# Kernel optimization log

Measured on AMD Instinct MI355X. Metric: run time of the kernel, lower is better.

The kernel has to match this reference:

```python
import jax, jax.numpy as jnp
import numpy as np

NUM_HEADS = 16
HEAD_DIM = 128
ROTARY_DIM = 32  # head_dim * rotary_pct(0.25)
ROPE_BASE = 10000.0
SCALE = HEAD_DIM ** -0.5


def _rotate_half(x):
    x1, x2 = jnp.split(x, 2, axis=-1)
    return jnp.concatenate((-x2, x1), axis=-1)


def _rope_tables(seq_len, dtype):
    inv_freq = 1.0 / (ROPE_BASE ** (jnp.arange(0, ROTARY_DIM, 2, dtype=jnp.float32) / ROTARY_DIM))
    freqs = jnp.arange(seq_len, dtype=jnp.float32)[:, None] * inv_freq[None, :]  # [S, rd/2]
    emb = jnp.concatenate((freqs, freqs), axis=-1)  # [S, rd]
    return jnp.cos(emb).astype(dtype), jnp.sin(emb).astype(dtype)


def setup_inputs() -> dict:
    key = jax.random.key(0)
    k1, k2, k3 = jax.random.split(key, 3)
    B, S, H = 2, 2048, 2048
    hidden_states = jax.random.normal(k1, (B, S, H), dtype=jnp.float32)
    attention_mask = jnp.zeros((B, 1, S, S), dtype=jnp.float32)
    Wqkv = jax.random.normal(k2, (H, 3 * H), dtype=jnp.float32) * (H ** -0.5)
    Wout = jax.random.normal(k3, (H, H), dtype=jnp.float32) * (H ** -0.5)
    return {"hidden_states": hidden_states, "attention_mask": attention_mask,
            "Wqkv": Wqkv, "Wout": Wout}


def reference(hidden_states, attention_mask, Wqkv, Wout):
    B, S, H = hidden_states.shape
    qkv = jnp.einsum('bsh,hk->bsk', hidden_states, Wqkv)  # [B,S,3H]
    q, k, v = jnp.split(qkv, 3, axis=-1)

    def to_heads(x):
        return x.reshape(B, S, NUM_HEADS, HEAD_DIM).transpose(0, 2, 1, 3)  # [B,nh,S,hd]

    q, k, v = to_heads(q), to_heads(k), to_heads(v)

    cos, sin = _rope_tables(S, hidden_states.dtype)  # [S, ROTARY_DIM]
    cos = cos[None, None, :, :]
    sin = sin[None, None, :, :]

    def rope(x):
        xr = x[..., :ROTARY_DIM]
        xr = xr * cos + _rotate_half(xr) * sin
        return jnp.concatenate((xr, x[..., ROTARY_DIM:]), axis=-1)

    q, k = rope(q), rope(k)

    scores = jnp.einsum('bhqd,bhkd->bhqk', q, k) * SCALE + attention_mask
    probs = jax.nn.softmax(scores, axis=-1)  # dropout p=0 -> identity
    ctx = jnp.einsum('bhqk,bhkd->bhqd', probs, v)
    ctx = ctx.transpose(0, 2, 1, 3).reshape(B, S, H)
    return jnp.einsum('bsh,ho->bso', ctx, Wout)
```

## Files before the change

### kernel.cpp

```cpp
#include <hip/hip_runtime.h>

typedef __attribute__((ext_vector_type(4))) float f32x4;
typedef __attribute__((ext_vector_type(8))) short s16x8;
typedef __attribute__((ext_vector_type(4))) unsigned short u16x4;
typedef __attribute__((ext_vector_type(8))) unsigned short u16x8;

#define DEVINL __device__ __forceinline__

constexpr int Bb = 2;
constexpr int Ss = 2048;
constexpr int Hh = 2048;
constexpr int NH = 16;
constexpr int HD = 128;
constexpr float ATT_SCALE = 0.08838834764831845f;
constexpr float CEXP = ATT_SCALE * 1.44269504089f;
constexpr float INV_SCALE = 11.313708498984761f;
constexpr float RAW_THR = 90.50966799f;

DEVINL unsigned short f2bf(float f) {
    unsigned u = __float_as_uint(f);
    u += 0x7FFFu + ((u >> 16) & 1u);
    return (unsigned short)(u >> 16);
}
DEVINL float bf2f(unsigned short h) { return __uint_as_float(((unsigned)h) << 16); }
DEVINL float fexp2(float x) { return __builtin_amdgcn_exp2f(x); }

DEVINL void gl16(const void* g, void* l) {
    __builtin_amdgcn_global_load_lds((const __attribute__((address_space(1))) void*)g,
                                     (__attribute__((address_space(3))) void*)l, 16, 0, 0);
}

__global__ void zero_flag_k(int* f) { if (threadIdx.x == 0) *f = 0; }

__global__ void scan_mask_k(const float* __restrict__ m, int* __restrict__ flag) {
    size_t i = ((size_t)blockIdx.x * 256 + threadIdx.x) * 4;
    f32x4 v = *(const f32x4*)(m + i);
    int any = (v[0] != 0.f) || (v[1] != 0.f) || (v[2] != 0.f) || (v[3] != 0.f);
    if (__any(any)) { if ((threadIdx.x & 63) == 0) atomicOr(flag, 1); }
}

__global__ void convH_k(const float* __restrict__ x, unsigned short* __restrict__ y) {
    size_t i = (size_t)blockIdx.x * 256 + threadIdx.x;
    f32x4 a = *(const f32x4*)(x + i * 8);
    f32x4 b = *(const f32x4*)(x + i * 8 + 4);
    u16x8 o;
    o[0] = f2bf(a[0]); o[1] = f2bf(a[1]); o[2] = f2bf(a[2]); o[3] = f2bf(a[3]);
    o[4] = f2bf(b[0]); o[5] = f2bf(b[1]); o[6] = f2bf(b[2]); o[7] = f2bf(b[3]);
    *(u16x8*)(y + i * 8) = o;
}

__global__ void convT_k(const float* __restrict__ W, unsigned short* __restrict__ Wt,
                        int R, int C) {
    __shared__ float tile[32][33];
    int c0 = blockIdx.x * 32, r0 = blockIdx.y * 32;
    int t = threadIdx.x;
    int rr = t >> 3, cc = (t & 7) * 4;
    f32x4 v = *(const f32x4*)(W + (size_t)(r0 + rr) * C + c0 + cc);
    tile[rr][cc + 0] = v[0]; tile[rr][cc + 1] = v[1];
    tile[rr][cc + 2] = v[2]; tile[rr][cc + 3] = v[3];
    __syncthreads();
    u16x4 o;
    o[0] = f2bf(tile[cc + 0][rr]); o[1] = f2bf(tile[cc + 1][rr]);
    o[2] = f2bf(tile[cc + 2][rr]); o[3] = f2bf(tile[cc + 3][rr]);
    *(u16x4*)(Wt + (size_t)(c0 + rr) * R + r0 + cc) = o;
}

#define PH(buf, kh, ih, sbuf, sunit, st, vm)                                      \
  {                                                                               \
    const char* Ar = lds + (buf)*65536;                                           \
    const char* Br = Ar + 32768;                                                  \
    s16x8 af[4];                                                                  \
    if ((ih) == 0) {                                                              \
      _Pragma("unroll")                                                           \
      for (int j = 0; j < 4; ++j) {                                               \
        int row = wn*64 + j*16 + lr;                                              \
        bfr[j] = *(const s16x8*)(Br + row*128 + (((kh)*64 + lg*16) ^ ((row&7)<<4))); \
      }                                                                           \
    }                                                                             \
    _Pragma("unroll")                                                             \
    for (int i = 0; i < 4; ++i) {                                                 \
      int row = wm*128 + (ih)*64 + i*16 + lr;                                     \
      af[i] = *(const s16x8*)(Ar + row*128 + (((kh)*64 + lg*16) ^ ((row&7)<<4))); \
    }                                                                             \
    STG(sbuf, sunit, st);                                                         \
    __builtin_amdgcn_s_barrier();                                                 \
    __builtin_amdgcn_sched_barrier(0);                                            \
    asm volatile("s_waitcnt lgkmcnt(0)" ::: "memory");                            \
    __builtin_amdgcn_sched_barrier(0);                                            \
    __builtin_amdgcn_s_setprio(1);                                                \
    _Pragma("unroll")                                                             \
    for (int i = 0; i < 4; ++i)                                                   \
      _Pragma("unroll")                                                           \
      for (int j = 0; j < 4; ++j)                                                 \
        acc[(ih)*4 + i][j] = __builtin_amdgcn_mfma_f32_16x16x32_bf16(             \
            af[i], bfr[j], acc[(ih)*4 + i][j], 0, 0, 0);                          \
    __builtin_amdgcn_s_setprio(0);                                                \
    if ((vm) >= 0) { asm volatile("s_waitcnt vmcnt(2)" ::: "memory"); }           \
    __builtin_amdgcn_sched_barrier(0);                                            \
    __builtin_amdgcn_s_barrier();                                                 \
    __builtin_amdgcn_sched_barrier(0);                                            \
  }

template<int MODE>
__global__ __launch_bounds__(512, 2)
void gemm256_k(const unsigned short* __restrict__ A, const unsigned short* __restrict__ Bt,
               float* __restrict__ Cf, unsigned short* __restrict__ Cb,
               int M, int N, int K) {
    __shared__ char lds[131072];
    int t = threadIdx.x, w = t >> 6, ln = t & 63, lr = ln & 15, lg = ln >> 4;
    int wm = w >> 2, wn = w & 3;
    int f = blockIdx.x, cpx = gridDim.x >> 3;
    int s = (f & 7) * cpx + (f >> 3);
    int nbn = N >> 8;
    int nb = s % nbn, mb = s / nbn;
    int m0 = mb * 256, n0 = nb * 256;
    const char* Ab = (const char*)A;
    const char* Bbp = (const char*)Bt;

    f32x4 acc[8][4];
#pragma unroll
    for (int i = 0; i < 8; ++i)
#pragma unroll
        for (int j = 0; j < 4; ++j) { acc[i][j][0] = 0.f; acc[i][j][1] = 0.f; acc[i][j][2] = 0.f; acc[i][j][3] = 0.f; }

    auto STG = [&](int sbuf, int unit, int kt) {
        int isB = unit >> 1;
        const char* src = isB ? Bbp : Ab;
        int rbase = isB ? n0 : m0;
        char* reg = lds + sbuf * 65536 + isB * 32768;
        size_t kb = ((size_t)kt * 64) * 2;
#pragma unroll
        for (int rr = 0; rr < 2; ++rr) {
            int rowbase = isB ? ((unit & 1) * 128 + rr * 64)
                              : (rr * 128 + (unit & 1) * 64);
            int row = rowbase + (t >> 3);
            int slot = (t & 7) ^ (row & 7);
            gl16(src + ((size_t)(rbase + row) * K) * 2 + kb + slot * 16,
                 reg + rowbase * 128 + t * 16);
        }
    };

    const int NT = K >> 6;
    STG(0, 0, 0); STG(0, 2, 0); STG(0, 3, 0); STG(0, 1, 0);
    STG(1, 0, 1);
    asm volatile("s_waitcnt vmcnt(2)" ::: "memory");
    __builtin_amdgcn_sched_barrier(0);
    __builtin_amdgcn_s_barrier();
    __builtin_amdgcn_sched_barrier(0);

    s16x8 bfr[4];
    for (int it = 0; it < (NT >> 1); ++it) {
        int e = it * 2;
        int e2 = (e + 2 < NT) ? e + 2 : e;
        int e3 = (e + 3 < NT) ? e + 3 : e + 1;
        PH(0, 0, 0,  1, 2, e + 1, -1)
        PH(0, 0, 1,  1, 3, e + 1, -1)
        PH(0, 1, 0,  1, 1, e + 1, -1)
        PH(0, 1, 1,  0, 0, e2,    1)
        PH(1, 0, 0,  0, 2, e2,   -1)
        PH(1, 0, 1,  0, 3, e2,   -1)
        PH(1, 1, 0,  0, 1, e2,   -1)
        PH(1, 1, 1,  1, 0, e3,    1)
    }
    asm volatile("s_waitcnt vmcnt(0)" ::: "memory");

    if (MODE == 0 && n0 < 4096 && (wn & 1) == 0) {
        float invf = fexp2((float)lr * -0.83048202372f);
#pragma unroll
        for (int i = 0; i < 8; ++i)
#pragma unroll
            for (int r = 0; r < 4; ++r) {
                int srow = (m0 + wm * 128 + i * 16 + lg * 4 + r) & (Ss - 1);
                float sn, cs;
                sincosf((float)srow * invf, &sn, &cs);
                float x1 = acc[i][0][r], x2 = acc[i][1][r];
                acc[i][0][r] = x1 * cs - x2 * sn;
                acc[i][1][r] = x2 * cs + x1 * sn;
            }
    }

#pragma unroll
    for (int i = 0; i < 8; ++i)
#pragma unroll
        for (int j = 0; j < 4; ++j)
#pragma unroll
            for (int r = 0; r < 4; ++r) {
                int gr = m0 + wm * 128 + i * 16 + lg * 4 + r;
                int gc = n0 + wn * 64 + j * 16 + lr;
                float vv = acc[i][j][r];
                if (MODE == 1) Cf[(size_t)gr * N + gc] = vv;
                else           Cb[(size_t)gr * N + gc] = f2bf(vv);
            }
}

__global__ void vtrans_k(const unsigned short* __restrict__ qkv, unsigned short* __restrict__ Vt) {
    __shared__ unsigned short tile[64][40];
    int bh = blockIdx.x; int b = bh >> 4, h = bh & 15;
    int s0 = blockIdx.y * 64, d0 = blockIdx.z * 32;
    int t = threadIdx.x;
    int r = t >> 2, c8 = (t & 3) * 8;
    u16x8 v = *(const u16x8*)(qkv + ((size_t)(b * Ss + s0 + r)) * 6144 + 4096 + h * 128 + d0 + c8);
#pragma unroll
    for (int e = 0; e < 8; ++e) tile[r][c8 + e] = v[e];
    __syncthreads();
    int dr = t >> 3, sc = (t & 7) * 8;
    u16x8 o;
#pragma unroll
    for (int e = 0; e < 8; ++e) o[e] = tile[sc + e][dr];
    *(u16x8*)(Vt + ((size_t)bh * HD + d0 + dr) * Ss + s0 + sc) = o;
}

__global__ __launch_bounds__(512)
void attn_k(const unsigned short* __restrict__ qkv, const unsigned short* __restrict__ Vt,
            const float* __restrict__ mask, unsigned short* __restrict__ ctxb,
            const int* __restrict__ flag) {
    __shared__ char ldsK[64 * 256];
    __shared__ char ldsV[128 * 128];
    __shared__ unsigned short ldsP[8][1024];
    int f = blockIdx.x;
    int swzb = (f & 7) * 64 + (f >> 3);
    int bh = swzb >> 4, qt = swzb & 15;
    int b = bh >> 4, h = bh & 15;
    int t = threadIdx.x, w = t >> 6, ln = t & 63, lr = ln & 15, lg = ln >> 4;
    int useMask = *flag;
    int qw0 = qt * 128 + w * 16;
    const char* qkvB = (const char*)qkv;
    const char* VtB = (const char*)Vt;

    s16x8 qf[4];
    size_t qbase = ((size_t)(b * Ss + qw0 + lr)) * 6144 + h * 128;
#pragma unroll
    for (int kc = 0; kc < 4; ++kc) qf[kc] = *(const s16x8*)(qkv + qbase + kc * 32 + lg * 8);

    float mr = -3e38f, lsum = 0.f;
    f32x4 ctxa[8];
#pragma unroll
    for (int dn = 0; dn < 8; ++dn) { ctxa[dn][0] = 0.f; ctxa[dn][1] = 0.f; ctxa[dn][2] = 0.f; ctxa[dn][3] = 0.f; }
    const float* mrow = mask + (size_t)b * Ss * Ss;

    for (int kk0 = 0; kk0 < Ss; kk0 += 64) {
        __syncthreads();
#pragma unroll
        for (int c = 0; c < 2; ++c) {
            int ci = c * 512 + t;
            int krow = ci >> 4, kcb = (ci & 15) << 4;
            gl16(qkvB + (((size_t)(b * Ss + kk0 + krow)) * 6144 + 2048 + h * 128) * 2 + (kcb ^ ((krow & 7) << 4)),
                 ldsK + ci * 16);
            int vrow = ci >> 3, vcb = (ci & 7) << 4;
            gl16(VtB + (((size_t)(bh * 128 + vrow)) * 2048 + kk0) * 2 + (vcb ^ ((vrow & 7) << 4)),
                 ldsV + ci * 16);
        }
        __syncthreads();

        f32x4 st[4];
#pragma unroll
        for (int n = 0; n < 4; ++n) {
            f32x4 sacc = {0.f, 0.f, 0.f, 0.f};
            const char* kb = ldsK + (n * 16 + lr) * 256;
            int sw = (lr & 7) << 4;
#pragma unroll
            for (int kc = 0; kc < 4; ++kc) {
                s16x8 kf = *(const s16x8*)(kb + ((kc * 64 + lg * 16) ^ sw));
                sacc = __builtin_amdgcn_mfma_f32_16x16x32_bf16(kf, qf[kc], sacc, 0, 0, 0);
            }
            st[n] = sacc;
        }
        if (useMask) {
#pragma unroll
            for (int n = 0; n < 4; ++n)
#pragma unroll
                for (int r = 0; r < 4; ++r)
                    st[n][r] += mrow[(size_t)(qw0 + lr) * Ss + kk0 + n * 16 + lg * 4 + r] * INV_SCALE;
        }
        float pmax = st[0][0];
#pragma unroll
        for (int n = 0; n < 4; ++n)
#pragma unroll
            for (int r = 0; r < 4; ++r) pmax = fmaxf(pmax, st[n][r]);
        pmax = fmaxf(pmax, __shfl_xor(pmax, 16));
        pmax = fmaxf(pmax, __shfl_xor(pmax, 32));
        bool need = pmax > mr + RAW_THR;
        if (__any(need)) {
            float mn = fmaxf(mr, pmax);
            float al = fexp2((mr - mn) * CEXP);
            mr = mn;
            lsum *= al;
            float a0 = __shfl(al, lg * 4 + 0), a1 = __shfl(al, lg * 4 + 1);
            float a2 = __shfl(al, lg * 4 + 2), a3 = __shfl(al, lg * 4 + 3);
#pragma unroll
            for (int dn = 0; dn < 8; ++dn) {
                ctxa[dn][0] *= a0; ctxa[dn][1] *= a1; ctxa[dn][2] *= a2; ctxa[dn][3] *= a3;
            }
        }
        float mC = mr * CEXP;
        float rs = 0.f;
        u16x4 pk[4];
#pragma unroll
        for (int n = 0; n < 4; ++n)
#pragma unroll
            for (int r = 0; r < 4; ++r) {
                float p = fexp2(st[n][r] * CEXP - mC);
                rs += p;
                pk[n][r] = f2bf(p);
            }
        rs += __shfl_xor(rs, 16);
        rs += __shfl_xor(rs, 32);
        lsum += rs;
        char* pw = (char*)ldsP[w];
        int swp = (lr & 7) << 4;
#pragma unroll
        for (int n = 0; n < 4; ++n)
            *(u16x4*)(pw + lr * 128 + ((32 * n + 8 * lg) ^ swp)) = pk[n];
        asm volatile("s_waitcnt lgkmcnt(0)" ::: "memory");
        s16x8 pa[2];
#pragma unroll
        for (int c2 = 0; c2 < 2; ++c2)
            pa[c2] = *(const s16x8*)(pw + lr * 128 + ((64 * c2 + 16 * lg) ^ swp));
#pragma unroll
        for (int dn = 0; dn < 8; ++dn) {
            const char* vb = ldsV + (dn * 16 + lr) * 128;
#pragma unroll
            for (int c2 = 0; c2 < 2; ++c2) {
                s16x8 vf = *(const s16x8*)(vb + ((c2 * 64 + lg * 16) ^ swp));
                ctxa[dn] = __builtin_amdgcn_mfma_f32_16x16x32_bf16(pa[c2], vf, ctxa[dn], 0, 0, 0);
            }
        }
    }
    float l0 = 1.f / __shfl(lsum, lg * 4 + 0), l1 = 1.f / __shfl(lsum, lg * 4 + 1);
    float l2 = 1.f / __shfl(lsum, lg * 4 + 2), l3 = 1.f / __shfl(lsum, lg * 4 + 3);
#pragma unroll
    for (int dn = 0; dn < 8; ++dn) {
        size_t base = ((size_t)(b * Ss + qw0)) * Hh + h * 128 + dn * 16 + lr;
        ctxb[base + (size_t)(lg * 4 + 0) * Hh] = f2bf(ctxa[dn][0] * l0);
        ctxb[base + (size_t)(lg * 4 + 1) * Hh] = f2bf(ctxa[dn][1] * l1);
        ctxb[base + (size_t)(lg * 4 + 2) * Hh] = f2bf(ctxa[dn][2] * l2);
        ctxb[base + (size_t)(lg * 4 + 3) * Hh] = f2bf(ctxa[dn][3] * l3);
    }
}

extern "C" void kernel_launch(void* const* d_in, const int* in_sizes, int n_in,
                              void* d_out, int out_size, void* d_ws, size_t ws_size,
                              hipStream_t stream) {
    (void)in_sizes; (void)n_in; (void)out_size; (void)ws_size;
    const float* hidden = (const float*)d_in[0];
    const float* mask   = (const float*)d_in[1];
    const float* Wqkv   = (const float*)d_in[2];
    const float* Wout   = (const float*)d_in[3];
    float* out = (float*)d_out;

    char* ws = (char*)d_ws;
    size_t off = 0;
    auto alloc = [&](size_t bytes) { char* p = ws + off; off += (bytes + 255) & ~(size_t)255; return p; };
    unsigned short* hbf   = (unsigned short*)alloc((size_t)8388608 * 2);
    unsigned short* wqkvT = (unsigned short*)alloc((size_t)12582912 * 2);
    unsigned short* woutT = (unsigned short*)alloc((size_t)4194304 * 2);
    unsigned short* qkv   = (unsigned short*)alloc((size_t)25165824 * 2);
    unsigned short* Vt    = (unsigned short*)alloc((size_t)8388608 * 2);
    int* flag             = (int*)alloc(256);
    unsigned short* ctx = hbf;

    zero_flag_k<<<1, 64, 0, stream>>>(flag);
    scan_mask_k<<<2048, 256, 0, stream>>>(mask, flag);
    convH_k<<<4096, 256, 0, stream>>>(hidden, hbf);
    convT_k<<<dim3(192, 64), 256, 0, stream>>>(Wqkv, wqkvT, 2048, 6144);
    convT_k<<<dim3(64, 64), 256, 0, stream>>>(Wout, woutT, 2048, 2048);
    gemm256_k<0><<<384, 512, 0, stream>>>(hbf, wqkvT, nullptr, qkv, 4096, 6144, 2048);
    vtrans_k<<<dim3(32, 32, 4), 256, 0, stream>>>(qkv, Vt);
    attn_k<<<512, 512, 0, stream>>>(qkv, Vt, mask, ctx, flag);
    gemm256_k<1><<<128, 512, 0, stream>>>(ctx, woutT, out, nullptr, 4096, 2048, 2048);
}
```

Before: 317.6 us.

## Use 128x128-tile GEMM for output projection and drop sched barriers

Adds a simpler 128x128-tile, 256-thread bf16 MFMA GEMM and uses it for the output projection. The grid grows from 128 to 512 blocks, which should fill the GPU's compute units better than the 256x256 tile did. The new kernel is not double-buffered and syncs each k-step, so load latency is exposed. Separately, it removes the sched_barrier fences around waits and barriers in the large GEMM, handing instruction ordering back to the compiler.

```diff
diff --git a/kernel.cpp b/kernel.cpp
--- a/kernel.cpp
+++ b/kernel.cpp
@@ -84,9 +84,7 @@
     }                                                                             \
     STG(sbuf, sunit, st);                                                         \
     __builtin_amdgcn_s_barrier();                                                 \
-    __builtin_amdgcn_sched_barrier(0);                                            \
     asm volatile("s_waitcnt lgkmcnt(0)" ::: "memory");                            \
-    __builtin_amdgcn_sched_barrier(0);                                            \
     __builtin_amdgcn_s_setprio(1);                                                \
     _Pragma("unroll")                                                             \
     for (int i = 0; i < 4; ++i)                                                   \
@@ -96,9 +94,7 @@
             af[i], bfr[j], acc[(ih)*4 + i][j], 0, 0, 0);                          \
     __builtin_amdgcn_s_setprio(0);                                                \
     if ((vm) >= 0) { asm volatile("s_waitcnt vmcnt(2)" ::: "memory"); }           \
-    __builtin_amdgcn_sched_barrier(0);                                            \
     __builtin_amdgcn_s_barrier();                                                 \
-    __builtin_amdgcn_sched_barrier(0);                                            \
   }
 
 template<int MODE>
@@ -144,9 +140,7 @@
     STG(0, 0, 0); STG(0, 2, 0); STG(0, 3, 0); STG(0, 1, 0);
     STG(1, 0, 1);
     asm volatile("s_waitcnt vmcnt(2)" ::: "memory");
-    __builtin_amdgcn_sched_barrier(0);
     __builtin_amdgcn_s_barrier();
-    __builtin_amdgcn_sched_barrier(0);
 
     s16x8 bfr[4];
     for (int it = 0; it < (NT >> 1); ++it) {
@@ -187,6 +181,73 @@
             for (int r = 0; r < 4; ++r) {
                 int gr = m0 + wm * 128 + i * 16 + lg * 4 + r;
                 int gc = n0 + wn * 64 + j * 16 + lr;
+                float vv = acc[i][j][r];
+                if (MODE == 1) Cf[(size_t)gr * N + gc] = vv;
+                else           Cb[(size_t)gr * N + gc] = f2bf(vv);
+            }
+}
+
+template<int MODE>
+__global__ __launch_bounds__(256)
+void gemm_bt_k(const unsigned short* __restrict__ A, const unsigned short* __restrict__ Bt,
+               float* __restrict__ Cf, unsigned short* __restrict__ Cb,
+               int M, int N, int K) {
+    __shared__ char lds[128 * 64 * 2 * 2];
+    char* As = lds;
+    char* Bs = lds + 128 * 64 * 2;
+    int t = threadIdx.x, w = t >> 6, ln = t & 63, lr = ln & 15, lg = ln >> 4;
+    int f = blockIdx.x;
+    int cpx = gridDim.x >> 3;
+    int s = (f & 7) * cpx + (f >> 3);
+    int nbn = N >> 7;
+    int nb = s % nbn, mb = s / nbn;
+    int m0 = mb * 128, n0 = nb * 128;
+    int wr = w >> 1, wc = w & 1;
+    const char* Abt = (const char*)A;
+    const char* Bbt = (const char*)Bt;
+
+    f32x4 acc[4][4];
+#pragma unroll
+    for (int i = 0; i < 4; ++i)
+#pragma unroll
+        for (int j = 0; j < 4; ++j) { acc[i][j][0] = 0.f; acc[i][j][1] = 0.f; acc[i][j][2] = 0.f; acc[i][j][3] = 0.f; }
+
+    for (int k0 = 0; k0 < K; k0 += 64) {
+        __syncthreads();
+#pragma unroll
+        for (int vv = 0; vv < 4; ++vv) {
+            int ci = vv * 256 + t;
+            int row = ci >> 3, cb = (ci & 7) << 4;
+            int sc = cb ^ ((row & 7) << 4);
+            gl16(Abt + ((size_t)(m0 + row) * K + k0) * 2 + sc, As + ci * 16);
+            gl16(Bbt + ((size_t)(n0 + row) * K + k0) * 2 + sc, Bs + ci * 16);
+        }
+        __syncthreads();
+#pragma unroll
+        for (int kc = 0; kc < 2; ++kc) {
+            s16x8 af[4], bfr[4];
+#pragma unroll
+            for (int i = 0; i < 4; ++i) {
+                int rowa = wr * 64 + i * 16 + lr;
+                af[i] = *(const s16x8*)(As + rowa * 128 + ((kc * 64 + lg * 16) ^ ((rowa & 7) << 4)));
+                int rowb = wc * 64 + i * 16 + lr;
+                bfr[i] = *(const s16x8*)(Bs + rowb * 128 + ((kc * 64 + lg * 16) ^ ((rowb & 7) << 4)));
+            }
+#pragma unroll
+            for (int i = 0; i < 4; ++i)
+#pragma unroll
+                for (int j = 0; j < 4; ++j)
+                    acc[i][j] = __builtin_amdgcn_mfma_f32_16x16x32_bf16(af[i], bfr[j], acc[i][j], 0, 0, 0);
+        }
+    }
+#pragma unroll
+    for (int i = 0; i < 4; ++i)
+#pragma unroll
+        for (int j = 0; j < 4; ++j)
+#pragma unroll
+            for (int r = 0; r < 4; ++r) {
+                int gr = m0 + wr * 64 + i * 16 + lg * 4 + r;
+                int gc = n0 + wc * 64 + j * 16 + lr;
                 float vv = acc[i][j][r];
                 if (MODE == 1) Cf[(size_t)gr * N + gc] = vv;
                 else           Cb[(size_t)gr * N + gc] = f2bf(vv);
@@ -367,5 +428,5 @@
     gemm256_k<0><<<384, 512, 0, stream>>>(hbf, wqkvT, nullptr, qkv, 4096, 6144, 2048);
     vtrans_k<<<dim3(32, 32, 4), 256, 0, stream>>>(qkv, Vt);
     attn_k<<<512, 512, 0, stream>>>(qkv, Vt, mask, ctx, flag);
-    gemm256_k<1><<<128, 512, 0, stream>>>(ctx, woutT, out, nullptr, 4096, 2048, 2048);
-}
+    gemm_bt_k<1><<<512, 256, 0, stream>>>(ctx, woutT, out, nullptr, 4096, 2048, 2048);
+}
```

Measured after the change: 308.7 us. -2.8%, faster.
